# Kernel tuning notes

Measured on AMD Instinct MI355X. Metric: run time of the kernel, lower is better.

## Reference

```python
import jax, jax.numpy as jnp
import numpy as np

DIM = 384
H_RES, W_RES = 56, 56
HEADS = 12
WS = 7          # window size
SS = 3          # shift size
N = WS * WS     # tokens per window
NW = (H_RES // WS) * (W_RES // WS)
EPS = 1e-5


def _rel_pos_index(ws):
    coords = np.stack(np.meshgrid(np.arange(ws), np.arange(ws), indexing='ij'))  # [2,ws,ws]
    cf = coords.reshape(2, -1)                      # [2, N]
    rc = (cf[:, :, None] - cf[:, None, :]).transpose(1, 2, 0)  # [N,N,2]
    rc[..., 0] += ws - 1
    rc[..., 1] += ws - 1
    rc[..., 0] *= 2 * ws - 1
    return rc.sum(-1)                               # [N,N] int


def _attn_mask(h, w, ws, ss):
    img = np.zeros((h, w))
    cnt = 0
    slices = (slice(0, -ws), slice(-ws, -ss), slice(-ss, None))
    for hs in slices:
        for wsl in slices:
            img[hs, wsl] = cnt
            cnt += 1
    mw = img.reshape(h // ws, ws, w // ws, ws).transpose(0, 2, 1, 3).reshape(-1, ws * ws)  # [nW,N]
    d = mw[:, None, :] - mw[:, :, None]
    return np.where(d != 0, -100.0, 0.0).astype(np.float32)  # [nW,N,N]


RPI = jnp.asarray(_rel_pos_index(WS).reshape(-1))          # [N*N]
ATTN_MASK = jnp.asarray(_attn_mask(H_RES, W_RES, WS, SS))  # [nW,N,N]


def _layernorm(x, g, b):
    mu = jnp.mean(x, axis=-1, keepdims=True)
    var = jnp.mean(jnp.square(x - mu), axis=-1, keepdims=True)
    return (x - mu) * jax.lax.rsqrt(var + EPS) * g + b


def setup_inputs() -> dict:
    key = jax.random.key(0)
    ks = jax.random.split(key, 8)
    s = 0.02
    return {
        'x': jax.random.normal(ks[0], (32, 1 + H_RES * W_RES, DIM), jnp.float32),
        'norm1_g': jnp.ones((DIM,), jnp.float32),
        'norm1_b': jnp.zeros((DIM,), jnp.float32),
        'qkv_w': jax.random.normal(ks[1], (DIM, 3 * DIM), jnp.float32) * s,
        'qkv_b': jnp.zeros((3 * DIM,), jnp.float32),
        'rpb_table': jax.random.normal(ks[2], ((2 * WS - 1) ** 2, HEADS), jnp.float32) * s,
        'proj_w': jax.random.normal(ks[3], (DIM, DIM), jnp.float32) * s,
        'proj_b': jnp.zeros((DIM,), jnp.float32),
        'norm2_g': jnp.ones((DIM,), jnp.float32),
        'norm2_b': jnp.zeros((DIM,), jnp.float32),
        'fc1_w': jax.random.normal(ks[4], (DIM, 4 * DIM), jnp.float32) * s,
        'fc1_b': jnp.zeros((4 * DIM,), jnp.float32),
        'fc2_w': jax.random.normal(ks[5], (4 * DIM, DIM), jnp.float32) * s,
        'fc2_b': jnp.zeros((DIM,), jnp.float32),
    }


def reference(x, norm1_g, norm1_b, qkv_w, qkv_b, rpb_table, proj_w, proj_b,
              norm2_g, norm2_b, fc1_w, fc1_b, fc2_w, fc2_b):
    B = x.shape[0]
    C = DIM
    hd = C // HEADS
    scale = hd ** -0.5

    time_token = x[:, :1, :]          # [B,1,C]
    img = x[:, 1:, :]                 # [B,H*W,C]
    shortcut = img

    h = _layernorm(img, norm1_g, norm1_b).reshape(B, H_RES, W_RES, C)
    h = jnp.roll(h, shift=(-SS, -SS), axis=(1, 2))  # cyclic shift

    # window partition -> [B*nW, N, C]
    xw = h.reshape(B, H_RES // WS, WS, W_RES // WS, WS, C)
    xw = xw.transpose(0, 1, 3, 2, 4, 5).reshape(-1, N, C)

    # window attention
    qkv = (xw @ qkv_w + qkv_b).reshape(-1, N, 3, HEADS, hd).transpose(2, 0, 3, 1, 4)
    q, k, v = qkv[0], qkv[1], qkv[2]                 # [B*nW, H, N, hd]
    attn = jnp.einsum('whnd,whmd->whnm', q * scale, k)
    bias = rpb_table[RPI].reshape(N, N, HEADS).transpose(2, 0, 1)  # [H,N,N]
    attn = attn + bias[None]
    attn = attn.reshape(B, NW, HEADS, N, N) + ATTN_MASK[None, :, None]
    attn = jax.nn.softmax(attn.reshape(-1, HEADS, N, N), axis=-1)
    out = jnp.einsum('whnm,whmd->wnhd', attn, v).reshape(-1, N, C)
    out = out @ proj_w + proj_b

    # window reverse -> [B,H,W,C]
    out = out.reshape(B, H_RES // WS, W_RES // WS, WS, WS, C)
    out = out.transpose(0, 1, 3, 2, 4, 5).reshape(B, H_RES, W_RES, C)
    out = jnp.roll(out, shift=(SS, SS), axis=(1, 2)).reshape(B, H_RES * W_RES, C)

    img = shortcut + out
    x = jnp.concatenate([time_token, img], axis=1)   # [B,1+H*W,C]
    x = _layernorm(x, norm2_g, norm2_b)
    hmlp = jax.nn.gelu(x @ fc1_w + fc1_b, approximate=False)
    x = x + (hmlp @ fc2_w + fc2_b)
    return x
```

## Files before the change

### kernel.cpp

```cpp
#include <hip/hip_runtime.h>
#include <hip/hip_bf16.h>

#define DIM 384
#define HEADS 12
#define NTOK 49
#define TOKENS 3137
#define M_ATTN 100352
#define M_FULL 100384
#define M_PAD2 100608
#define SCALEQ 0.17677669529663687f

typedef __attribute__((ext_vector_type(8))) short s8v;
typedef __attribute__((ext_vector_type(4))) float f4v;
typedef unsigned short u16;

__device__ __forceinline__ float b2f(int s) {
  union { unsigned u; float f; } c; c.u = ((unsigned)(s & 0xffff)) << 16; return c.f;
}
__device__ __forceinline__ u16 f2b(float f) {
  __hip_bfloat16 h = __float2bfloat16(f);
  return *reinterpret_cast<u16*>(&h);
}
__device__ __forceinline__ void gload16(const void* g, void* l) {
  __builtin_amdgcn_global_load_lds((const __attribute__((address_space(1))) void*)g,
                                   (__attribute__((address_space(3))) void*)l, 16, 0, 0);
}
__device__ __forceinline__ float gelu_f(float val) {
  float u = __builtin_fmaf(0.0713548163f * val, val * val, 1.5957691216f * val);
  return val * __builtin_amdgcn_rcpf(1.0f + __expf(-u));
}
__device__ __forceinline__ size_t tidx(int tile, int KS, int rl, int c) {
  return ((size_t)(tile * KS + (c >> 6)) * 128 + rl) * 64
       + (((((c >> 3) & 7)) ^ (rl & 7)) << 3) + (c & 7);
}

__global__ void k_convert(const float* __restrict__ qkv_w, const float* __restrict__ qkv_b,
                          const float* __restrict__ proj_w, const float* __restrict__ proj_b,
                          const float* __restrict__ fc1_w, const float* __restrict__ fc1_b,
                          const float* __restrict__ fc2_w, const float* __restrict__ fc2_b,
                          u16* __restrict__ wt_qkv, float* __restrict__ qkvb_s,
                          u16* __restrict__ wt_proj, float* __restrict__ projb_s,
                          u16* __restrict__ wt_fc1, float* __restrict__ fc1b_s,
                          u16* __restrict__ wt_fc2, float* __restrict__ fc2b_s) {
  int i = blockIdx.x * 256 + threadIdx.x;
  if (i < 1152 * 384) { int n = i / 384, k = i % 384;
    float v = qkv_w[(size_t)k * 1152 + n]; if (n < 384) v *= SCALEQ;
    wt_qkv[tidx(n >> 7, 6, n & 127, k)] = f2b(v); }
  if (i < 128 * 384) { int n = 1152 + i / 384, k = i % 384;
    wt_qkv[tidx(n >> 7, 6, n & 127, k)] = 0; }
  if (i < 1280) qkvb_s[i] = (i < 1152) ? qkv_b[i] * (i < 384 ? SCALEQ : 1.0f) : 0.0f;
  if (i < 384 * 384) { int n = i / 384, k = i % 384;
    wt_proj[tidx(n >> 7, 6, n & 127, k)] = f2b(proj_w[(size_t)k * 384 + n]); }
  if (i < 128 * 384) { int n = 384 + i / 384, k = i % 384;
    wt_proj[tidx(n >> 7, 6, n & 127, k)] = 0; }
  if (i < 512) projb_s[i] = (i < 384) ? proj_b[i] : 0.0f;
  if (i < 1536 * 384) { int n = i / 384, k = i % 384;
    wt_fc1[tidx(n >> 7, 6, n & 127, k)] = f2b(fc1_w[(size_t)k * 1536 + n]); }
  if (i < 1536) fc1b_s[i] = fc1_b[i];
  if (i < 384 * 1536) { int n = i / 1536, k = i % 1536;
    wt_fc2[tidx(n >> 7, 24, n & 127, k)] = f2b(fc2_w[(size_t)k * 384 + n]); }
  if (i < 128 * 1536) { int n = 384 + i / 1536, k = i % 1536;
    wt_fc2[tidx(n >> 7, 24, n & 127, k)] = 0; }
  if (i < 512) fc2b_s[i] = (i < 384) ? fc2_b[i] : 0.0f;
}

__global__ void k_addtab(const float* __restrict__ rpb, float* __restrict__ ADD) {
  int idx = blockIdx.x * 256 + threadIdx.x;
  if (idx >= 4 * HEADS * NTOK * NTOK) return;
  int j = idx % NTOK, t = idx / NTOK;
  int i = t % NTOK; t /= NTOK;
  int h = t % HEADS; int cls = t / HEADS;
  int ii = i / 7, jj = i % 7, ji = j / 7, j2 = j % 7;
  int rpi = (ii - ji + 6) * 13 + (jj - j2 + 6);
  float v = rpb[rpi * HEADS + h];
  int rh = (cls & 2) ? (ii < 4 ? 1 : 2) : 0;
  int rw = (cls & 1) ? (jj < 4 ? 1 : 2) : 0;
  int sh = (cls & 2) ? (ji < 4 ? 1 : 2) : 0;
  int sw = (cls & 1) ? (j2 < 4 ? 1 : 2) : 0;
  if (rh != sh || rw != sw) v -= 100.0f;
  ADD[idx] = v;
}

__global__ void k_ln1(const float* __restrict__ x, const float* __restrict__ g,
                      const float* __restrict__ b, u16* __restrict__ xwt, int t0) {
  int wid = threadIdx.x >> 6, lane = threadIdx.x & 63;
  int ml = blockIdx.x * 4 + wid;
  int t = t0 + ml;
  int bi = t / 3136, rem = t % 3136;
  int win = rem / NTOK, n = rem % NTOK;
  int wh = win >> 3, ww = win & 7, ii = n / 7, jj = n % 7;
  int h = (wh * 7 + ii + 3) % 56;
  int w = (ww * 7 + jj + 3) % 56;
  const float* src = x + ((size_t)bi * TOKENS + 1 + h * 56 + w) * DIM;
  float v[6];
  #pragma unroll
  for (int e = 0; e < 6; e++) v[e] = src[lane + e * 64];
  float s = v[0] + v[1] + v[2] + v[3] + v[4] + v[5];
  #pragma unroll
  for (int m = 1; m < 64; m <<= 1) s += __shfl_xor(s, m);
  float mu = s * (1.0f / 384.0f);
  float q = 0.f;
  #pragma unroll
  for (int e = 0; e < 6; e++) { float d = v[e] - mu; q += d * d; }
  #pragma unroll
  for (int m = 1; m < 64; m <<= 1) q += __shfl_xor(q, m);
  float rstd = rsqrtf(q * (1.0f / 384.0f) + 1e-5f);
  int tile = ml >> 7, rl = ml & 127;
  #pragma unroll
  for (int e = 0; e < 6; e++) {
    int c = lane + e * 64;
    xwt[tidx(tile, 6, rl, c)] = f2b((v[e] - mu) * rstd * g[c] + b[c]);
  }
}

template<int MODE>
__global__ __launch_bounds__(512, 2) void k_gemm256(
    const u16* __restrict__ At, const u16* __restrict__ Bt,
    const float* __restrict__ bias, u16* __restrict__ Cb,
    float* __restrict__ outp, const u16* __restrict__ residt,
    int Nreal, int KT, int row_off) {
  __shared__ __align__(16) u16 Ls[2][4][8192];
  int gx = gridDim.x;
  int lid = blockIdx.y * gx + blockIdx.x;
  int nwg = gx * gridDim.y;
  int q = nwg >> 3, r = nwg & 7;
  int xcd = lid & 7, loc = lid >> 3;
  int tile = (xcd < r ? xcd * (q + 1) : r * (q + 1) + (xcd - r) * q) + loc;
  int m0 = (tile / gx) * 256, n0 = (tile % gx) * 256;
  int tid = threadIdx.x;
  int wid = tid >> 6, lane = tid & 63;
  int lo = lane & 15, hi = lane >> 4;
  int wm = wid >> 2, wn = wid & 3;
  int cidx = wid >> 1, half = wid & 1;
  const u16* gsrc = (cidx < 2)
      ? At + ((size_t)((m0 >> 7) + cidx) * KT) * 8192
      : Bt + ((size_t)((n0 >> 7) + (cidx - 2)) * KT) * 8192;
  gsrc += half * 4096 + lane * 8;
  f4v acc[8][4];
  #pragma unroll
  for (int mi = 0; mi < 8; mi++)
    #pragma unroll
    for (int ni = 0; ni < 4; ni++) acc[mi][ni] = (f4v)(0.0f);
#define STG(buf, kt) do {                                                \
    u16* d_ = &Ls[buf][cidx][half * 4096];                               \
    const u16* s_ = gsrc + (size_t)(kt) * 8192;                          \
    _Pragma("unroll")                                                    \
    for (int g_ = 0; g_ < 8; g_++) gload16(s_ + g_ * 512, d_ + g_ * 512);\
  } while (0)
  STG(0, 0);
  for (int kt = 0; kt < KT; ++kt) {
    int c = kt & 1;
    if (kt + 1 < KT) {
      STG(1 - c, kt + 1);
      asm volatile("s_waitcnt vmcnt(8)" ::: "memory");
    } else {
      asm volatile("s_waitcnt vmcnt(0)" ::: "memory");
    }
    __builtin_amdgcn_s_barrier();
    __builtin_amdgcn_sched_barrier(0);
    #pragma unroll
    for (int kk = 0; kk < 2; kk++) {
      int kk4 = kk * 4;
      s8v af[8], bf[4];
      #pragma unroll
      for (int mi = 0; mi < 8; mi++) {
        int rl = mi * 16 + lo;
        af[mi] = *(const s8v*)(&Ls[c][wm][rl * 64 + (((kk4 + hi) ^ (rl & 7)) << 3)]);
      }
      #pragma unroll
      for (int ni = 0; ni < 4; ni++) {
        int rb = (wn & 1) * 64 + ni * 16 + lo;
        bf[ni] = *(const s8v*)(&Ls[c][2 + (wn >> 1)][rb * 64 + (((kk4 + hi) ^ (rb & 7)) << 3)]);
      }
      asm volatile("s_waitcnt lgkmcnt(0)" ::: "memory");
      __builtin_amdgcn_sched_barrier(0);
      if (kk == 1) {
        __builtin_amdgcn_s_barrier();
        __builtin_amdgcn_sched_barrier(0);
      }
      __builtin_amdgcn_s_setprio(1);
      #pragma unroll
      for (int mi = 0; mi < 8; mi++)
        #pragma unroll
        for (int ni = 0; ni < 4; ni++)
          acc[mi][ni] = __builtin_amdgcn_mfma_f32_16x16x32_bf16(af[mi], bf[ni], acc[mi][ni], 0, 0, 0);
      __builtin_amdgcn_s_setprio(0);
    }
  }
#undef STG
  #pragma unroll
  for (int mi = 0; mi < 8; mi++)
    #pragma unroll
    for (int ni = 0; ni < 4; ni++) {
      int gcol = n0 + wn * 64 + ni * 16 + lo;
      float bv = bias[gcol];
      #pragma unroll
      for (int r2 = 0; r2 < 4; r2++) {
        int grow = m0 + wm * 128 + mi * 16 + hi * 4 + r2;
        float val = acc[mi][ni][r2] + bv;
        if (MODE == 0) {
          if (gcol < Nreal) Cb[(size_t)grow * Nreal + gcol] = f2b(val);
        } else if (MODE == 1) {
          Cb[tidx(grow >> 7, 24, grow & 127, gcol)] = f2b(gelu_f(val));
        } else {
          int orow = grow + row_off;
          if (orow < M_FULL && gcol < Nreal) {
            float res = b2f(residt[tidx(orow >> 7, 6, orow & 127, gcol)]);
            outp[(size_t)orow * 384 + gcol] = val + res;
          }
        }
      }
    }
}

__global__ __launch_bounds__(256) void k_attn2(const u16* __restrict__ qkv,
                                               const float* __restrict__ ADD,
                                               u16* __restrict__ aot, int win0) {
  __shared__ u16 PT[4][64][76];
  __shared__ u16 VT[4][32][76];
  int wid = threadIdx.x >> 6, lane = threadIdx.x & 63;
  int lo = lane & 15, hi = lane >> 4;
  int gw = blockIdx.x * 4 + wid;
  int win_l = gw / HEADS, h = gw % HEADS;
  int nw = (win0 + win_l) & 63;
  int wh = nw >> 3, ww = nw & 7;
  int cls = ((wh == 7) ? 2 : 0) + ((ww == 7) ? 1 : 0);
  size_t rowbase = (size_t)win_l * NTOK;
  u16 (*pt)[76] = PT[wid];
  u16 (*vt)[76] = VT[wid];

  int rcl[4];
  #pragma unroll
  for (int ti = 0; ti < 4; ti++) {
    int r = ti * 16 + lo;
    rcl[ti] = r < NTOK ? r : NTOK - 1;
  }
  int jrow = lane < NTOK ? lane : NTOK - 1;

  s8v af[4], bf[4];
  #pragma unroll
  for (int ti = 0; ti < 4; ti++) {
    af[ti] = *(const s8v*)(qkv + (rowbase + rcl[ti]) * 1152 + h * 32 + hi * 8);
    bf[ti] = *(const s8v*)(qkv + (rowbase + rcl[ti]) * 1152 + 384 + h * 32 + hi * 8);
  }
  f4v st[4][4];
  #pragma unroll
  for (int mi = 0; mi < 4; mi++)
    #pragma unroll
    for (int ni = 0; ni < 4; ni++)
      st[mi][ni] = __builtin_amdgcn_mfma_f32_16x16x32_bf16(af[mi], bf[ni], (f4v)(0.0f), 0, 0, 0);

  {
    const u16* vsrc = qkv + (rowbase + jrow) * 1152 + 768 + h * 32;
    #pragma unroll
    for (int d0 = 0; d0 < 32; d0 += 8) {
      s8v v = *(const s8v*)(vsrc + d0);
      #pragma unroll
      for (int e = 0; e < 8; e++) vt[d0 + e][lane] = (u16)v[e];
    }
  }

  const float* addb = ADD + ((size_t)cls * HEADS + h) * (NTOK * NTOK);
  #pragma unroll
  for (int mi = 0; mi < 4; mi++)
    #pragma unroll
    for (int ni = 0; ni < 4; ni++) {
      int jj = ni * 16 + lo;
      #pragma unroll
      for (int r = 0; r < 4; r++) {
        int i = mi * 16 + hi * 4 + r;
        if (jj < NTOK) {
          int ic = i < NTOK ? i : NTOK - 1;
          st[mi][ni][r] += addb[ic * NTOK + jj];
        } else st[mi][ni][r] = -1e30f;
      }
    }

  float invl[4][4];
  #pragma unroll
  for (int mi = 0; mi < 4; mi++)
    #pragma unroll
    for (int r = 0; r < 4; r++) {
      float m = fmaxf(fmaxf(st[mi][0][r], st[mi][1][r]), fmaxf(st[mi][2][r], st[mi][3][r]));
      #pragma unroll
      for (int msk = 1; msk < 16; msk <<= 1) m = fmaxf(m, __shfl_xor(m, msk));
      float s = 0.f;
      #pragma unroll
      for (int ni = 0; ni < 4; ni++) {
        float p = __expf(st[mi][ni][r] - m);
        st[mi][ni][r] = p;
        s += p;
      }
      #pragma unroll
      for (int msk = 1; msk < 16; msk <<= 1) s += __shfl_xor(s, msk);
      invl[mi][r] = 1.0f / s;
    }

  #pragma unroll
  for (int ni = 0; ni < 4; ni++)
    #pragma unroll
    for (int mi = 0; mi < 4; mi++) {
      ushort4 pk;
      pk.x = f2b(st[mi][ni][0]); pk.y = f2b(st[mi][ni][1]);
      pk.z = f2b(st[mi][ni][2]); pk.w = f2b(st[mi][ni][3]);
      *(ushort4*)(&pt[ni * 16 + lo][mi * 16 + hi * 4]) = pk;
    }

  f4v ot[4][2];
  #pragma unroll
  for (int mi = 0; mi < 4; mi++)
    #pragma unroll
    for (int dt = 0; dt < 2; dt++) ot[mi][dt] = (f4v)(0.0f);
  #pragma unroll
  for (int kt = 0; kt < 2; kt++) {
    s8v pa[4], vb[2];
    #pragma unroll
    for (int mi = 0; mi < 4; mi++) {
      s8v p;
      #pragma unroll
      for (int e = 0; e < 8; e++) p[e] = (short)pt[kt * 32 + hi * 8 + e][mi * 16 + lo];
      pa[mi] = p;
    }
    #pragma unroll
    for (int dt = 0; dt < 2; dt++) {
      short4 a = *(const short4*)(&vt[dt * 16 + lo][kt * 32 + hi * 8]);
      short4 b = *(const short4*)(&vt[dt * 16 + lo][kt * 32 + hi * 8 + 4]);
      s8v v; v[0] = a.x; v[1] = a.y; v[2] = a.z; v[3] = a.w;
             v[4] = b.x; v[5] = b.y; v[6] = b.z; v[7] = b.w;
      vb[dt] = v;
    }
    #pragma unroll
    for (int mi = 0; mi < 4; mi++)
      #pragma unroll
      for (int dt = 0; dt < 2; dt++)
        ot[mi][dt] = __builtin_amdgcn_mfma_f32_16x16x32_bf16(pa[mi], vb[dt], ot[mi][dt], 0, 0, 0);
  }

  #pragma unroll
  for (int mi = 0; mi < 4; mi++)
    #pragma unroll
    for (int r = 0; r < 4; r++) {
      int i = mi * 16 + hi * 4 + r;
      if (i < NTOK) {
        int row = (int)rowbase + i;
        int tile = row >> 7, rl = row & 127;
        aot[tidx(tile, 6, rl, h * 32 + lo)]      = f2b(ot[mi][0][r] * invl[mi][r]);
        aot[tidx(tile, 6, rl, h * 32 + 16 + lo)] = f2b(ot[mi][1][r] * invl[mi][r]);
      }
    }
}

__global__ void k_ln2(const float* __restrict__ x, const u16* __restrict__ proj,
                      const float* __restrict__ g, const float* __restrict__ b,
                      u16* __restrict__ x2bt) {
  int wid = threadIdx.x >> 6, lane = threadIdx.x & 63;
  int r = blockIdx.x * 4 + wid;
  int tile = r >> 7, rl = r & 127;
  if (r >= M_FULL) {
    u16 z = f2b(0.0f);
    #pragma unroll
    for (int e = 0; e < 6; e++) x2bt[tidx(tile, 6, rl, lane + e * 64)] = z;
    return;
  }
  int bi = r / TOKENS, tk = r % TOKENS;
  const float* xs = x + (size_t)r * DIM;
  float v[6];
  if (tk == 0) {
    #pragma unroll
    for (int e = 0; e < 6; e++) v[e] = xs[lane + e * 64];
  } else {
    int p = tk - 1, hh = p / 56, wp = p % 56;
    int a = (hh + 53) % 56, bw = (wp + 53) % 56;
    int wh = a / 7, ii = a % 7, w2 = bw / 7, jj = bw % 7;
    size_t prow = ((size_t)bi * 64 + wh * 8 + w2) * NTOK + ii * 7 + jj;
    const u16* ps = proj + prow * DIM;
    #pragma unroll
    for (int e = 0; e < 6; e++) v[e] = xs[lane + e * 64] + b2f(ps[lane + e * 64]);
  }
  float s = v[0] + v[1] + v[2] + v[3] + v[4] + v[5];
  #pragma unroll
  for (int m = 1; m < 64; m <<= 1) s += __shfl_xor(s, m);
  float mu = s * (1.0f / 384.0f);
  float q = 0.f;
  #pragma unroll
  for (int e = 0; e < 6; e++) { float d = v[e] - mu; q += d * d; }
  #pragma unroll
  for (int m = 1; m < 64; m <<= 1) q += __shfl_xor(q, m);
  float rstd = rsqrtf(q * (1.0f / 384.0f) + 1e-5f);
  #pragma unroll
  for (int e = 0; e < 6; e++) {
    int c = lane + e * 64;
    x2bt[tidx(tile, 6, rl, c)] = f2b((v[e] - mu) * rstd * g[c] + b[c]);
  }
}

extern "C" void kernel_launch(void* const* d_in, const int* in_sizes, int n_in,
                              void* d_out, int out_size, void* d_ws, size_t ws_size,
                              hipStream_t stream) {
  const float* x      = (const float*)d_in[0];
  const float* n1g    = (const float*)d_in[1];
  const float* n1b    = (const float*)d_in[2];
  const float* qkv_w  = (const float*)d_in[3];
  const float* qkv_b  = (const float*)d_in[4];
  const float* rpb    = (const float*)d_in[5];
  const float* proj_w = (const float*)d_in[6];
  const float* proj_b = (const float*)d_in[7];
  const float* n2g    = (const float*)d_in[8];
  const float* n2b    = (const float*)d_in[9];
  const float* fc1_w  = (const float*)d_in[10];
  const float* fc1_b  = (const float*)d_in[11];
  const float* fc2_w  = (const float*)d_in[12];
  const float* fc2_b  = (const float*)d_in[13];
  float* outp = (float*)d_out;

  auto al = [](size_t v) { return (v + 255) & ~(size_t)255; };
  size_t base = al(983040) + al(393216) + al(1179648) + al(1572864)
              + al(5120) + al(2048) + al(6144) + al(2048)
              + al(460992) + al((size_t)M_PAD2 * 768)
              + al((size_t)M_ATTN * 768);
  const int cand[5][2] = {{1, 1}, {1, 2}, {2, 3}, {4, 6}, {8, 12}};
  int NC1 = 8, NC2 = 12;
  for (int ci = 0; ci < 5; ci++) {
    int c1 = cand[ci][0], c2 = cand[ci][1];
    size_t cm = M_ATTN / c1;
    int ct = (393 + c2 - 1) / c2;
    size_t qf = cm * 2304;
    size_t fc1b = (size_t)ct * 786432;
    if (fc1b > qf) qf = fc1b;
    size_t tot = base + al(cm * 768) + al(qf);
    if (tot <= ws_size) { NC1 = c1; NC2 = c2; break; }
  }
  char* p = (char*)d_ws;
  auto take = [&](size_t bytes) { char* r = p; p += al(bytes); return r; };
  u16* wt_qkv  = (u16*)take(983040);
  u16* wt_proj = (u16*)take(393216);
  u16* wt_fc1  = (u16*)take(1179648);
  u16* wt_fc2  = (u16*)take(1572864);
  float* qkvb_s = (float*)take(5120);
  float* projb_s = (float*)take(2048);
  float* fc1b_s = (float*)take(6144);
  float* fc2b_s = (float*)take(2048);
  float* ADDt   = (float*)take(460992);
  u16* X2Bt = (u16*)take((size_t)M_PAD2 * 768);
  u16* PROJ = (u16*)take((size_t)M_ATTN * 768);
  int chunkM = M_ATTN / NC1;
  int ct = (393 + NC2 - 1) / NC2;
  u16* XWt  = (u16*)take((size_t)chunkM * 768);
  size_t qf = (size_t)chunkM * 2304;
  size_t fc1b = (size_t)ct * 786432;
  if (fc1b > qf) qf = fc1b;
  u16* QKV  = (u16*)take(qf);
  u16* AOt  = XWt;
  u16* FC1t = QKV;

  k_convert<<<2304, 256, 0, stream>>>(qkv_w, qkv_b, proj_w, proj_b, fc1_w, fc1_b,
                                      fc2_w, fc2_b, wt_qkv, qkvb_s, wt_proj, projb_s,
                                      wt_fc1, fc1b_s, wt_fc2, fc2b_s);
  k_addtab<<<451, 256, 0, stream>>>(rpb, ADDt);
  int chunkWin = chunkM / NTOK;
  int mt1 = chunkM / 256;
  for (int c = 0; c < NC1; c++) {
    int t0 = c * chunkM;
    k_ln1<<<chunkM / 4, 256, 0, stream>>>(x, n1g, n1b, XWt, t0);
    k_gemm256<0><<<dim3(5, mt1), 512, 0, stream>>>(XWt, wt_qkv, qkvb_s, QKV,
                                                   nullptr, nullptr, 1152, 6, 0);
    k_attn2<<<chunkWin * HEADS / 4, 256, 0, stream>>>(QKV, ADDt, AOt, c * chunkWin);
    k_gemm256<0><<<dim3(2, mt1), 512, 0, stream>>>(AOt, wt_proj, projb_s,
                                                   PROJ + (size_t)t0 * DIM,
                                                   nullptr, nullptr, 384, 6, 0);
  }
  k_ln2<<<M_PAD2 / 4, 256, 0, stream>>>(x, PROJ, n2g, n2b, X2Bt);
  for (int c = 0; c < NC2; c++) {
    int tb0 = c * ct;
    int nt = 393 - tb0; if (nt > ct) nt = ct; if (nt <= 0) break;
    k_gemm256<1><<<dim3(6, nt), 512, 0, stream>>>(
        X2Bt + (size_t)(tb0 * 2) * 6 * 8192, wt_fc1, fc1b_s, FC1t,
        nullptr, nullptr, 1536, 6, 0);
    k_gemm256<2><<<dim3(2, nt), 512, 0, stream>>>(
        FC1t, wt_fc2, fc2b_s, nullptr, outp, X2Bt, 384, 24, tb0 * 256);
  }
}
```

Before: 1.022 ms.

## Vectorize layernorms, stage GEMM epilogues through LDS, and reduce workspace chunk sizes

The two layernorm kernels now use float4 loads and ushort4 stores, and compute mean and variance in a single pass from sum and sum of squares. The GEMM epilogue writes accumulators into swizzled LDS and then emits coalesced 16-byte (bf16) or float4 (fp32 residual) global stores, where each lane previously stored scalars. The chunking candidates start at more chunks, which may keep per-chunk buffers L2/MALL-resident but adds launches. Risks are single-pass variance precision loss and extra barriers in the epilogue.

```diff
diff --git a/kernel.cpp b/kernel.cpp
--- a/kernel.cpp
+++ b/kernel.cpp
@@ -92,24 +92,36 @@
   int h = (wh * 7 + ii + 3) % 56;
   int w = (ww * 7 + jj + 3) % 56;
   const float* src = x + ((size_t)bi * TOKENS + 1 + h * 56 + w) * DIM;
-  float v[6];
-  #pragma unroll
-  for (int e = 0; e < 6; e++) v[e] = src[lane + e * 64];
-  float s = v[0] + v[1] + v[2] + v[3] + v[4] + v[5];
-  #pragma unroll
-  for (int m = 1; m < 64; m <<= 1) s += __shfl_xor(s, m);
+  bool a1 = lane < 32;
+  float4 v0 = *(const float4*)(src + lane * 4);
+  float4 v1 = a1 ? *(const float4*)(src + 256 + lane * 4) : float4{0, 0, 0, 0};
+  float s = v0.x + v0.y + v0.z + v0.w + v1.x + v1.y + v1.z + v1.w;
+  float ss = v0.x * v0.x + v0.y * v0.y + v0.z * v0.z + v0.w * v0.w
+           + v1.x * v1.x + v1.y * v1.y + v1.z * v1.z + v1.w * v1.w;
+  #pragma unroll
+  for (int m = 1; m < 64; m <<= 1) { s += __shfl_xor(s, m); ss += __shfl_xor(ss, m); }
   float mu = s * (1.0f / 384.0f);
-  float q = 0.f;
-  #pragma unroll
-  for (int e = 0; e < 6; e++) { float d = v[e] - mu; q += d * d; }
-  #pragma unroll
-  for (int m = 1; m < 64; m <<= 1) q += __shfl_xor(q, m);
-  float rstd = rsqrtf(q * (1.0f / 384.0f) + 1e-5f);
+  float rstd = rsqrtf(ss * (1.0f / 384.0f) - mu * mu + 1e-5f);
   int tile = ml >> 7, rl = ml & 127;
-  #pragma unroll
-  for (int e = 0; e < 6; e++) {
-    int c = lane + e * 64;
-    xwt[tidx(tile, 6, rl, c)] = f2b((v[e] - mu) * rstd * g[c] + b[c]);
+  {
+    int c0 = lane * 4;
+    float4 gg = *(const float4*)(g + c0), bb = *(const float4*)(b + c0);
+    ushort4 pk;
+    pk.x = f2b((v0.x - mu) * rstd * gg.x + bb.x);
+    pk.y = f2b((v0.y - mu) * rstd * gg.y + bb.y);
+    pk.z = f2b((v0.z - mu) * rstd * gg.z + bb.z);
+    pk.w = f2b((v0.w - mu) * rstd * gg.w + bb.w);
+    *(ushort4*)(&xwt[tidx(tile, 6, rl, c0)]) = pk;
+  }
+  if (a1) {
+    int c0 = 256 + lane * 4;
+    float4 gg = *(const float4*)(g + c0), bb = *(const float4*)(b + c0);
+    ushort4 pk;
+    pk.x = f2b((v1.x - mu) * rstd * gg.x + bb.x);
+    pk.y = f2b((v1.y - mu) * rstd * gg.y + bb.y);
+    pk.z = f2b((v1.z - mu) * rstd * gg.z + bb.z);
+    pk.w = f2b((v1.w - mu) * rstd * gg.w + bb.w);
+    *(ushort4*)(&xwt[tidx(tile, 6, rl, c0)]) = pk;
   }
 }
 
@@ -188,29 +200,85 @@
     }
   }
 #undef STG
-  #pragma unroll
-  for (int mi = 0; mi < 8; mi++)
-    #pragma unroll
-    for (int ni = 0; ni < 4; ni++) {
-      int gcol = n0 + wn * 64 + ni * 16 + lo;
-      float bv = bias[gcol];
-      #pragma unroll
-      for (int r2 = 0; r2 < 4; r2++) {
-        int grow = m0 + wm * 128 + mi * 16 + hi * 4 + r2;
-        float val = acc[mi][ni][r2] + bv;
-        if (MODE == 0) {
-          if (gcol < Nreal) Cb[(size_t)grow * Nreal + gcol] = f2b(val);
-        } else if (MODE == 1) {
-          Cb[tidx(grow >> 7, 24, grow & 127, gcol)] = f2b(gelu_f(val));
-        } else {
-          int orow = grow + row_off;
-          if (orow < M_FULL && gcol < Nreal) {
-            float res = b2f(residt[tidx(orow >> 7, 6, orow & 127, gcol)]);
-            outp[(size_t)orow * 384 + gcol] = val + res;
+  u16* Lc = (u16*)Ls;
+  if (MODE == 0 || MODE == 1) {
+    #pragma unroll
+    for (int mi = 0; mi < 8; mi++)
+      #pragma unroll
+      for (int ni = 0; ni < 4; ni++) {
+        int lcol = wn * 64 + ni * 16 + lo;
+        float bv = bias[n0 + lcol];
+        #pragma unroll
+        for (int r2 = 0; r2 < 4; r2++) {
+          int lrow = wm * 128 + mi * 16 + hi * 4 + r2;
+          float val = acc[mi][ni][r2] + bv;
+          if (MODE == 0) {
+            Lc[lrow * 256 + (((lcol >> 3) ^ (lrow & 7)) << 3) + (lcol & 7)] = f2b(val);
+          } else {
+            Lc[(lrow >> 7) * 32768 + (lcol >> 6) * 8192 + (lrow & 127) * 64
+               + (((((lcol & 63) >> 3)) ^ (lrow & 7)) << 3) + (lcol & 7)] = f2b(gelu_f(val));
           }
         }
       }
-    }
+    __syncthreads();
+    if (MODE == 0) {
+      #pragma unroll
+      for (int it = 0; it < 16; it++) {
+        int idx = it * 512 + tid;
+        int row = idx >> 5, ck = idx & 31;
+        int gcol = n0 + ck * 8;
+        if (gcol < Nreal) {
+          s8v v = *(const s8v*)(Lc + row * 256 + ((ck ^ (row & 7)) << 3));
+          *(s8v*)(&Cb[(size_t)(m0 + row) * Nreal + gcol]) = v;
+        }
+      }
+    } else {
+      size_t b0 = ((size_t)((m0 >> 7) * 24) + (n0 >> 6)) * 8192;
+      size_t b1 = ((size_t)(((m0 >> 7) + 1) * 24) + (n0 >> 6)) * 8192;
+      #pragma unroll
+      for (int it = 0; it < 16; it++) {
+        int idx = it * 512 + tid;
+        s8v v = ((const s8v*)Lc)[idx];
+        u16* dst = (idx < 4096) ? (Cb + b0 + (size_t)idx * 8)
+                                : (Cb + b1 + (size_t)(idx - 4096) * 8);
+        *(s8v*)dst = v;
+      }
+    }
+  } else {
+    float* Lf = (float*)Ls;
+    for (int g2 = 0; g2 < 2; g2++) {
+      __syncthreads();
+      if (wm == g2) {
+        #pragma unroll
+        for (int mi = 0; mi < 8; mi++)
+          #pragma unroll
+          for (int ni = 0; ni < 4; ni++) {
+            int lcol = wn * 64 + ni * 16 + lo;
+            float bv = bias[n0 + lcol];
+            #pragma unroll
+            for (int r2 = 0; r2 < 4; r2++) {
+              int row = mi * 16 + hi * 4 + r2;
+              Lf[row * 256 + (((lcol >> 2) ^ (row & 7)) << 2) + (lcol & 3)]
+                  = acc[mi][ni][r2] + bv;
+            }
+          }
+      }
+      __syncthreads();
+      #pragma unroll
+      for (int it = 0; it < 16; it++) {
+        int idx = it * 512 + tid;
+        int row = idx >> 6, ck = idx & 63;
+        int orow = m0 + g2 * 128 + row + row_off;
+        int gcol = n0 + ck * 4;
+        if (orow < M_FULL && gcol < 384) {
+          float4 v = *(const float4*)(Lf + row * 256 + ((ck ^ (row & 7)) << 2));
+          ushort4 rs = *(const ushort4*)(&residt[tidx(orow >> 7, 6, orow & 127, gcol)]);
+          v.x += b2f(rs.x); v.y += b2f(rs.y); v.z += b2f(rs.z); v.w += b2f(rs.w);
+          *(float4*)(&outp[(size_t)orow * 384 + gcol]) = v;
+        }
+      }
+    }
+  }
 }
 
 __global__ __launch_bounds__(256) void k_attn2(const u16* __restrict__ qkv,
@@ -356,41 +424,57 @@
   int wid = threadIdx.x >> 6, lane = threadIdx.x & 63;
   int r = blockIdx.x * 4 + wid;
   int tile = r >> 7, rl = r & 127;
+  bool a1 = lane < 32;
   if (r >= M_FULL) {
-    u16 z = f2b(0.0f);
-    #pragma unroll
-    for (int e = 0; e < 6; e++) x2bt[tidx(tile, 6, rl, lane + e * 64)] = z;
+    ushort4 z = {0, 0, 0, 0};
+    z.x = z.y = z.z = z.w = f2b(0.0f);
+    *(ushort4*)(&x2bt[tidx(tile, 6, rl, lane * 4)]) = z;
+    if (a1) *(ushort4*)(&x2bt[tidx(tile, 6, rl, 256 + lane * 4)]) = z;
     return;
   }
   int bi = r / TOKENS, tk = r % TOKENS;
   const float* xs = x + (size_t)r * DIM;
-  float v[6];
-  if (tk == 0) {
-    #pragma unroll
-    for (int e = 0; e < 6; e++) v[e] = xs[lane + e * 64];
-  } else {
+  float4 v0 = *(const float4*)(xs + lane * 4);
+  float4 v1 = a1 ? *(const float4*)(xs + 256 + lane * 4) : float4{0, 0, 0, 0};
+  if (tk != 0) {
     int p = tk - 1, hh = p / 56, wp = p % 56;
     int a = (hh + 53) % 56, bw = (wp + 53) % 56;
     int wh = a / 7, ii = a % 7, w2 = bw / 7, jj = bw % 7;
     size_t prow = ((size_t)bi * 64 + wh * 8 + w2) * NTOK + ii * 7 + jj;
     const u16* ps = proj + prow * DIM;
-    #pragma unroll
-    for (int e = 0; e < 6; e++) v[e] = xs[lane + e * 64] + b2f(ps[lane + e * 64]);
-  }
-  float s = v[0] + v[1] + v[2] + v[3] + v[4] + v[5];
-  #pragma unroll
-  for (int m = 1; m < 64; m <<= 1) s += __shfl_xor(s, m);
+    ushort4 p0 = *(const ushort4*)(ps + lane * 4);
+    v0.x += b2f(p0.x); v0.y += b2f(p0.y); v0.z += b2f(p0.z); v0.w += b2f(p0.w);
+    if (a1) {
+      ushort4 p1 = *(const ushort4*)(ps + 256 + lane * 4);
+      v1.x += b2f(p1.x); v1.y += b2f(p1.y); v1.z += b2f(p1.z); v1.w += b2f(p1.w);
+    }
+  }
+  float s = v0.x + v0.y + v0.z + v0.w + v1.x + v1.y + v1.z + v1.w;
+  float ss = v0.x * v0.x + v0.y * v0.y + v0.z * v0.z + v0.w * v0.w
+           + v1.x * v1.x + v1.y * v1.y + v1.z * v1.z + v1.w * v1.w;
+  #pragma unroll
+  for (int m = 1; m < 64; m <<= 1) { s += __shfl_xor(s, m); ss += __shfl_xor(ss, m); }
   float mu = s * (1.0f / 384.0f);
-  float q = 0.f;
-  #pragma unroll
-  for (int e = 0; e < 6; e++) { float d = v[e] - mu; q += d * d; }
-  #pragma unroll
-  for (int m = 1; m < 64; m <<= 1) q += __shfl_xor(q, m);
-  float rstd = rsqrtf(q * (1.0f / 384.0f) + 1e-5f);
-  #pragma unroll
-  for (int e = 0; e < 6; e++) {
-    int c = lane + e * 64;
-    x2bt[tidx(tile, 6, rl, c)] = f2b((v[e] - mu) * rstd * g[c] + b[c]);
+  float rstd = rsqrtf(ss * (1.0f / 384.0f) - mu * mu + 1e-5f);
+  {
+    int c0 = lane * 4;
+    float4 gg = *(const float4*)(g + c0), bb = *(const float4*)(b + c0);
+    ushort4 pk;
+    pk.x = f2b((v0.x - mu) * rstd * gg.x + bb.x);
+    pk.y = f2b((v0.y - mu) * rstd * gg.y + bb.y);
+    pk.z = f2b((v0.z - mu) * rstd * gg.z + bb.z);
+    pk.w = f2b((v0.w - mu) * rstd * gg.w + bb.w);
+    *(ushort4*)(&x2bt[tidx(tile, 6, rl, c0)]) = pk;
+  }
+  if (a1) {
+    int c0 = 256 + lane * 4;
+    float4 gg = *(const float4*)(g + c0), bb = *(const float4*)(b + c0);
+    ushort4 pk;
+    pk.x = f2b((v1.x - mu) * rstd * gg.x + bb.x);
+    pk.y = f2b((v1.y - mu) * rstd * gg.y + bb.y);
+    pk.z = f2b((v1.z - mu) * rstd * gg.z + bb.z);
+    pk.w = f2b((v1.w - mu) * rstd * gg.w + bb.w);
+    *(ushort4*)(&x2bt[tidx(tile, 6, rl, c0)]) = pk;
   }
 }
 
@@ -418,7 +502,7 @@
               + al(5120) + al(2048) + al(6144) + al(2048)
               + al(460992) + al((size_t)M_PAD2 * 768)
               + al((size_t)M_ATTN * 768);
-  const int cand[5][2] = {{1, 1}, {1, 2}, {2, 3}, {4, 6}, {8, 12}};
+  const int cand[5][2] = {{2, 2}, {2, 3}, {4, 6}, {8, 12}, {16, 24}};
   int NC1 = 8, NC2 = 12;
   for (int ci = 0; ci < 5; ci++) {
     int c1 = cand[ci][0], c2 = cand[ci][1];
```

Measured after the change: 1.049 ms. 1.03x slower.
